# Optimization experiments

Hardware: AMD Instinct MI355X
Metric: run time of the kernel (lower is better)

Reference implementation:

```python
import jax, jax.numpy as jnp
import numpy as np

EPS = 1e-06


def setup_inputs() -> dict:
    key = jax.random.key(0)
    k1, k2 = jax.random.split(key)
    N, M, D = 8192, 8192, 512
    first_vector = jax.random.normal(k1, (N, D), dtype=jnp.float32)
    second_vector = jax.random.normal(k2, (M, D), dtype=jnp.float32)
    return {"first_vector": first_vector, "second_vector": second_vector, "normalize": 1}


def reference(first_vector, second_vector, normalize):
    # Pairwise dot products: [N, M]. Mathematically identical to the
    # broadcast multiply + sum over D in the torch module, but as a GEMM.
    sim = jnp.einsum('nd,md->nm', first_vector, second_vector)
    if normalize:
        # Note: module divides by sqrt(|a| * |b|) + eps (geometric mean of
        # norms, not the product) -- reproduce exactly.
        n1 = jnp.linalg.norm(first_vector, axis=1)[:, None]   # [N, 1]
        n2 = jnp.linalg.norm(second_vector, axis=1)[None, :]  # [1, M]
        sim = sim / (jnp.sqrt(n1 * n2) + EPS)
    return sim
```

## Files before the change

kernel.cpp:

```cpp
#include <hip/hip_runtime.h>
#include <hip/hip_bf16.h>
#include <math.h>

#define EPS 1e-6f

constexpr int D  = 512;
constexpr int BM = 256;
constexpr int BN = 256;

typedef __attribute__((ext_vector_type(8))) short  short8;
typedef __attribute__((ext_vector_type(4))) float  floatx4;

__device__ inline unsigned short f2bf(float f) {
  union { __hip_bfloat16 h; unsigned short u; } cvt;
  cvt.h = __float2bfloat16(f);
  return cvt.u;
}

__global__ __launch_bounds__(256) void prep_kernel(
    const float* __restrict__ src, __hip_bfloat16* __restrict__ dst,
    float* __restrict__ isn, int nrows) {
  const int lane = threadIdx.x & 63;
  const int row  = blockIdx.x * 4 + (threadIdx.x >> 6);
  if (row >= nrows) return;

  const float4* p4 = (const float4*)(src + (size_t)row * D);
  const float4 v1 = p4[lane];
  const float4 v2 = p4[lane + 64];

  if (dst != nullptr) {
    ushort4 u1, u2;
    u1.x = f2bf(v1.x); u1.y = f2bf(v1.y); u1.z = f2bf(v1.z); u1.w = f2bf(v1.w);
    u2.x = f2bf(v2.x); u2.y = f2bf(v2.y); u2.z = f2bf(v2.z); u2.w = f2bf(v2.w);
    ushort4* drow = (ushort4*)(dst + (size_t)row * D);
    drow[lane]      = u1;
    drow[lane + 64] = u2;
  }

  float ss = v1.x * v1.x + v1.y * v1.y + v1.z * v1.z + v1.w * v1.w
           + v2.x * v2.x + v2.y * v2.y + v2.z * v2.z + v2.w * v2.w;
  #pragma unroll
  for (int o = 32; o > 0; o >>= 1) ss += __shfl_down(ss, o);
  if (lane == 0) {
    const float n1 = sqrtf(ss);
    isn[row] = 1.0f / sqrtf(n1);
  }
}


#define GLD(srcp, ldsoff_shorts)                                              \
  __builtin_amdgcn_global_load_lds(                                           \
      (const __attribute__((address_space(1))) void*)(srcp),                  \
      (__attribute__((address_space(3))) void*)(smem + (ldsoff_shorts)),      \
      16, 0, 0)

#define STAGE_HALF(gbase, lbase)                                              \
  do {                                                                        \
    GLD((gbase) + soff,                   (lbase) + t * 8);                   \
    GLD((gbase) + soff + (size_t)64 * D,  (lbase) + (t + 512) * 8);           \
  } while (0)

#define STAGE_KTILE(kt, b)                                                    \
  do {                                                                        \
    STAGE_HALF(gA + (kt) * 64,                   ((b) * 2 + 0) * 8192);       \
    STAGE_HALF(gA + (kt) * 64 + (size_t)128 * D, ((b) * 2 + 1) * 8192);       \
    STAGE_HALF(gB + (kt) * 64,                   32768 + ((b) * 2 + 0) * 8192); \
    STAGE_HALF(gB + (kt) * 64 + (size_t)128 * D, 32768 + ((b) * 2 + 1) * 8192); \
  } while (0)

#define RD(p, m, off) (*(const short8*)((p) + (m) * 2048 + rbyte + (off)))

#define MM2(mi, ni)                                                           \
  do {                                                                        \
    acc[mi][ni] = __builtin_amdgcn_mfma_f32_16x16x32_bf16(                    \
        aR[(mi) & 3][0], bR[ni][0], acc[mi][ni], 0, 0, 0);                    \
    acc[mi][ni] = __builtin_amdgcn_mfma_f32_16x16x32_bf16(                    \
        aR[(mi) & 3][1], bR[ni][1], acc[mi][ni], 0, 0, 0);                    \
  } while (0)

#define BAR   __builtin_amdgcn_s_barrier()
#define LGKM0 do { asm volatile("s_waitcnt lgkmcnt(0)" ::: "memory");         \
                   __builtin_amdgcn_sched_barrier(0); } while (0)
#define VM8   asm volatile("s_waitcnt vmcnt(8)" ::: "memory")
#define VM0   asm volatile("s_waitcnt vmcnt(0)" ::: "memory")
#define NOOP  do {} while (0)

#define KTILE(b, STAGE_STMT, WAITV)                                           \
  do {                                                                        \
    const char* pA_ = (const char*)smem + ((b) * 2 + wm) * 16384;             \
    const char* pB_ = (const char*)smem + 65536                               \
                      + ((b) * 2 + (wn >> 1)) * 16384 + (wn & 1) * 8192;      \
                                 \
    aR[0][0] = RD(pA_, 0, off0); aR[0][1] = RD(pA_, 0, off1);                 \
    aR[1][0] = RD(pA_, 1, off0); aR[1][1] = RD(pA_, 1, off1);                 \
    aR[2][0] = RD(pA_, 2, off0); aR[2][1] = RD(pA_, 2, off1);                 \
    aR[3][0] = RD(pA_, 3, off0); aR[3][1] = RD(pA_, 3, off1);                 \
    bR[0][0] = RD(pB_, 0, off0); bR[0][1] = RD(pB_, 0, off1);                 \
    bR[1][0] = RD(pB_, 1, off0); bR[1][1] = RD(pB_, 1, off1);                 \
    BAR; LGKM0;                                                               \
    __builtin_amdgcn_s_setprio(1);                                            \
    MM2(0,0); MM2(1,0); MM2(2,0); MM2(3,0);                                   \
    MM2(0,1); MM2(1,1); MM2(2,1); MM2(3,1);                                   \
    __builtin_amdgcn_s_setprio(0);                                            \
    BAR;                                                                      \
                                                              \
    bR[2][0] = RD(pB_, 2, off0); bR[2][1] = RD(pB_, 2, off1);                 \
    bR[3][0] = RD(pB_, 3, off0); bR[3][1] = RD(pB_, 3, off1);                 \
    BAR; LGKM0;                                                               \
    __builtin_amdgcn_s_setprio(1);                                            \
    MM2(0,2); MM2(1,2); MM2(2,2); MM2(3,2);                                   \
    MM2(0,3); MM2(1,3); MM2(2,3); MM2(3,3);                                   \
    __builtin_amdgcn_s_setprio(0);                                            \
    BAR;                                                                      \
                                               \
    aR[0][0] = RD(pA_, 4, off0); aR[0][1] = RD(pA_, 4, off1);                 \
    aR[1][0] = RD(pA_, 5, off0); aR[1][1] = RD(pA_, 5, off1);                 \
    aR[2][0] = RD(pA_, 6, off0); aR[2][1] = RD(pA_, 6, off1);                 \
    aR[3][0] = RD(pA_, 7, off0); aR[3][1] = RD(pA_, 7, off1);                 \
    BAR; LGKM0;                                                               \
    __builtin_amdgcn_s_setprio(1);                                            \
    MM2(4,2); MM2(5,2); MM2(6,2); MM2(7,2);                                   \
    MM2(4,3); MM2(5,3); MM2(6,3); MM2(7,3);                                   \
    __builtin_amdgcn_s_setprio(0);                                            \
    BAR;                                                                      \
       \
    STAGE_STMT;                                                               \
    BAR;                                                                      \
    __builtin_amdgcn_s_setprio(1);                                            \
    MM2(4,0); MM2(5,0); MM2(6,0); MM2(7,0);                                   \
    MM2(4,1); MM2(5,1); MM2(6,1); MM2(7,1);                                   \
    __builtin_amdgcn_s_setprio(0);                                            \
    WAITV;                                                                    \
    BAR;                                                                      \
  } while (0)

__global__ __launch_bounds__(512, 2) void gemm256_kernel(
    const __hip_bfloat16* __restrict__ A, const __hip_bfloat16* __restrict__ B,
    const float* __restrict__ ia, const float* __restrict__ ib,
    const int* __restrict__ nrmflag, float* __restrict__ C,
    int N, int M) {
  __shared__ __align__(128) short smem[65536];

  const int t    = threadIdx.x;
  const int lane = t & 63;
  const int w    = t >> 6;
  const int wm   = w >> 2;
  const int wn   = w & 3;

  int bid = blockIdx.y * gridDim.x + blockIdx.x;
  const int nwg = (int)(gridDim.x * gridDim.y);
  if ((nwg & 7) == 0) bid = (bid & 7) * (nwg >> 3) + (bid >> 3);
  const int ix = bid % (int)gridDim.x;
  const int iy = bid / (int)gridDim.x;
  const size_t rowA0 = (size_t)ix * BM;
  const size_t rowB0 = (size_t)iy * BN;

  const int srow  = t >> 3;
  const int sslot = (t & 7) ^ (srow & 7);
  const size_t soff = (size_t)srow * D + sslot * 8;
  const unsigned short* gA = (const unsigned short*)A + rowA0 * D;
  const unsigned short* gB = (const unsigned short*)B + rowB0 * D;

  const int fr    = lane & 15;
  const int g4    = lane >> 4;
  const int rbyte = fr * 128;
  const int off0  = ((g4    ) ^ (fr & 7)) * 16;
  const int off1  = ((g4 + 4) ^ (fr & 7)) * 16;

  floatx4 acc[8][4];
  #pragma unroll
  for (int i = 0; i < 8; ++i)
    #pragma unroll
    for (int j = 0; j < 4; ++j) acc[i][j] = (floatx4){0.f, 0.f, 0.f, 0.f};

  short8 aR[4][2], bR[4][2];

  STAGE_KTILE(0, 0);
  STAGE_KTILE(1, 1);
  VM8;
  BAR;

  #pragma unroll
  for (int it = 0; it < 4; ++it) {
    if (it < 3) {
      KTILE(0, STAGE_KTILE(it * 2 + 2, 0), VM8);
      KTILE(1, STAGE_KTILE(it * 2 + 3, 1), VM8);
    } else {
      KTILE(0, NOOP, VM0);
      KTILE(1, NOOP, NOOP);
    }
  }

  const int nrm = *nrmflag;
  const int cq  = lane >> 4;
  const int cc  = lane & 15;

  float ibv[4];
  #pragma unroll
  for (int n = 0; n < 4; ++n)
    ibv[n] = nrm ? ib[rowB0 + wn * 64 + n * 16 + cc] : 1.0f;

  #pragma unroll
  for (int m = 0; m < 8; ++m) {
    const size_t rbase = rowA0 + wm * 128 + m * 16 + cq * 4;
    float4 iav4 = nrm ? *(const float4*)(ia + rbase) : (float4){1.f, 1.f, 1.f, 1.f};
    const float iavr[4] = {iav4.x, iav4.y, iav4.z, iav4.w};
    #pragma unroll
    for (int r = 0; r < 4; ++r) {
      float* crow = C + (rbase + r) * (size_t)M + rowB0 + wn * 64 + cc;
      #pragma unroll
      for (int n = 0; n < 4; ++n)
        crow[n * 16] = acc[m][n][r] * iavr[r] * ibv[n];
    }
  }
}

__global__ __launch_bounds__(256) void fb_gemm(
    const float* __restrict__ A, const float* __restrict__ B,
    const float* __restrict__ ia, const float* __restrict__ ib,
    const int* __restrict__ nrmflag, float* __restrict__ C, int N, int M) {
  __shared__ float sA[32][33];
  __shared__ float sB[32][33];
  const int tx = threadIdx.x & 31;
  const int ty = threadIdx.x >> 5;
  const size_t row0 = (size_t)blockIdx.y * 32;
  const size_t col0 = (size_t)blockIdx.x * 32;
  float acc[4] = {0.f, 0.f, 0.f, 0.f};
  for (int k0 = 0; k0 < D; k0 += 32) {
    #pragma unroll
    for (int r = 0; r < 4; ++r) {
      sA[ty + 8 * r][tx] = A[(row0 + ty + 8 * r) * D + k0 + tx];
      sB[ty + 8 * r][tx] = B[(col0 + ty + 8 * r) * D + k0 + tx];
    }
    __syncthreads();
    #pragma unroll 8
    for (int kk = 0; kk < 32; ++kk) {
      const float bv = sB[tx][kk];
      #pragma unroll
      for (int r = 0; r < 4; ++r) acc[r] += sA[ty + 8 * r][kk] * bv;
    }
    __syncthreads();
  }
  const int nrm  = *nrmflag;
  const float iv = ib[col0 + tx];
  #pragma unroll
  for (int r = 0; r < 4; ++r) {
    const size_t row = row0 + ty + 8 * r;
    float v = acc[r];
    if (nrm) {
      const float denom = 1.0f / (ia[row] * iv) + EPS;
      v /= denom;
    }
    C[row * (size_t)M + col0 + tx] = v;
  }
}

extern "C" void kernel_launch(void* const* d_in, const int* in_sizes, int n_in,
                              void* d_out, int out_size, void* d_ws, size_t ws_size,
                              hipStream_t stream) {
  const float* A   = (const float*)d_in[0];
  const float* B   = (const float*)d_in[1];
  const int*   nrm = (const int*)d_in[2];
  float*       C   = (float*)d_out;
  const int N = in_sizes[0] / D;
  const int M = in_sizes[1] / D;

  float* iaN = (float*)d_ws;
  float* ibN = iaN + N;
  __hip_bfloat16* Abf = (__hip_bfloat16*)(ibN + M);
  __hip_bfloat16* Bbf = Abf + (size_t)N * D;

  const size_t need = (size_t)(N + M) * sizeof(float)
                    + (size_t)(N + M) * D * sizeof(__hip_bfloat16);
  const bool fast = (ws_size >= need) && (N % BM == 0) && (M % BN == 0);

  prep_kernel<<<(N + 3) / 4, 256, 0, stream>>>(A, fast ? Abf : nullptr, iaN, N);
  prep_kernel<<<(M + 3) / 4, 256, 0, stream>>>(B, fast ? Bbf : nullptr, ibN, M);

  if (fast) {
    gemm256_kernel<<<dim3(N / BM, M / BN), 512, 0, stream>>>(Abf, Bbf, iaN, ibN, nrm, C, N, M);
  } else {
    fb_gemm<<<dim3(M / 32, N / 32), 256, 0, stream>>>(A, B, iaN, ibN, nrm, C, N, M);
  }
}
```

Measured before the change: 370.8 us.

## Persist GEMM blocks over four column tiles and fold norm scaling into bf16 prep

Each workgroup now computes four consecutive 256x256 output tiles along the M dimension. It prefetches the next tile's first k-slices during the tail of the current tile, which hides the pipeline fill and drain between tiles and reduces the grid size. The inverse-sqrt-norm scaling is applied to the bf16 operands in the prep kernel, so the GEMM epilogue becomes plain nontemporal stores with no ia/ib loads or multiplies. Pre-scaling before rounding to bf16 slightly changes numerics, and the launch has 4x fewer workgroups, which could under-fill the CUs.

```diff
diff --git a/kernel.cpp b/kernel.cpp
--- a/kernel.cpp
+++ b/kernel.cpp
@@ -4,9 +4,10 @@
 
 #define EPS 1e-6f
 
-constexpr int D  = 512;
-constexpr int BM = 256;
-constexpr int BN = 256;
+constexpr int D   = 512;
+constexpr int BM  = 256;
+constexpr int BN  = 256;
+constexpr int TPB = 4;
 
 typedef __attribute__((ext_vector_type(8))) short  short8;
 typedef __attribute__((ext_vector_type(4))) float  floatx4;
@@ -19,7 +20,7 @@
 
 __global__ __launch_bounds__(256) void prep_kernel(
     const float* __restrict__ src, __hip_bfloat16* __restrict__ dst,
-    float* __restrict__ isn, int nrows) {
+    float* __restrict__ isn, const int* __restrict__ nrmflag, int nrows) {
   const int lane = threadIdx.x & 63;
   const int row  = blockIdx.x * 4 + (threadIdx.x >> 6);
   if (row >= nrows) return;
@@ -28,22 +29,24 @@
   const float4 v1 = p4[lane];
   const float4 v2 = p4[lane + 64];
 
+  float ss = v1.x * v1.x + v1.y * v1.y + v1.z * v1.z + v1.w * v1.w
+           + v2.x * v2.x + v2.y * v2.y + v2.z * v2.z + v2.w * v2.w;
+  #pragma unroll
+  for (int o = 32; o > 0; o >>= 1) ss += __shfl_xor(ss, o);
+
+  const float s4 = rsqrtf(sqrtf(ss));
+  if (lane == 0) isn[row] = s4;
+
   if (dst != nullptr) {
+    const float s = (*nrmflag) ? s4 : 1.0f;
     ushort4 u1, u2;
-    u1.x = f2bf(v1.x); u1.y = f2bf(v1.y); u1.z = f2bf(v1.z); u1.w = f2bf(v1.w);
-    u2.x = f2bf(v2.x); u2.y = f2bf(v2.y); u2.z = f2bf(v2.z); u2.w = f2bf(v2.w);
+    u1.x = f2bf(v1.x * s); u1.y = f2bf(v1.y * s);
+    u1.z = f2bf(v1.z * s); u1.w = f2bf(v1.w * s);
+    u2.x = f2bf(v2.x * s); u2.y = f2bf(v2.y * s);
+    u2.z = f2bf(v2.z * s); u2.w = f2bf(v2.w * s);
     ushort4* drow = (ushort4*)(dst + (size_t)row * D);
     drow[lane]      = u1;
     drow[lane + 64] = u2;
-  }
-
-  float ss = v1.x * v1.x + v1.y * v1.y + v1.z * v1.z + v1.w * v1.w
-           + v2.x * v2.x + v2.y * v2.y + v2.z * v2.z + v2.w * v2.w;
-  #pragma unroll
-  for (int o = 32; o > 0; o >>= 1) ss += __shfl_down(ss, o);
-  if (lane == 0) {
-    const float n1 = sqrtf(ss);
-    isn[row] = 1.0f / sqrtf(n1);
   }
 }
 
@@ -54,18 +57,16 @@
       (__attribute__((address_space(3))) void*)(smem + (ldsoff_shorts)),      \
       16, 0, 0)
 
-#define STAGE_HALF(gbase, lbase)                                              \
-  do {                                                                        \
-    GLD((gbase) + soff,                   (lbase) + t * 8);                   \
-    GLD((gbase) + soff + (size_t)64 * D,  (lbase) + (t + 512) * 8);           \
-  } while (0)
-
-#define STAGE_KTILE(kt, b)                                                    \
-  do {                                                                        \
-    STAGE_HALF(gA + (kt) * 64,                   ((b) * 2 + 0) * 8192);       \
-    STAGE_HALF(gA + (kt) * 64 + (size_t)128 * D, ((b) * 2 + 1) * 8192);       \
-    STAGE_HALF(gB + (kt) * 64,                   32768 + ((b) * 2 + 0) * 8192); \
-    STAGE_HALF(gB + (kt) * 64 + (size_t)128 * D, 32768 + ((b) * 2 + 1) * 8192); \
+#define STAGE(aP, bP, b)                                                      \
+  do {                                                                        \
+    GLD((aP) + soff,                   ((b) * 2 + 0) * 8192 + t * 8);         \
+    GLD((aP) + soff + (size_t)64 * D,  ((b) * 2 + 0) * 8192 + (t + 512) * 8); \
+    GLD((aP) + soff + (size_t)128 * D, ((b) * 2 + 1) * 8192 + t * 8);         \
+    GLD((aP) + soff + (size_t)192 * D, ((b) * 2 + 1) * 8192 + (t + 512) * 8); \
+    GLD((bP) + soff,                   32768 + ((b) * 2 + 0) * 8192 + t * 8); \
+    GLD((bP) + soff + (size_t)64 * D,  32768 + ((b) * 2 + 0) * 8192 + (t + 512) * 8); \
+    GLD((bP) + soff + (size_t)128 * D, 32768 + ((b) * 2 + 1) * 8192 + t * 8); \
+    GLD((bP) + soff + (size_t)192 * D, 32768 + ((b) * 2 + 1) * 8192 + (t + 512) * 8); \
   } while (0)
 
 #define RD(p, m, off) (*(const short8*)((p) + (m) * 2048 + rbyte + (off)))
@@ -90,7 +91,7 @@
     const char* pA_ = (const char*)smem + ((b) * 2 + wm) * 16384;             \
     const char* pB_ = (const char*)smem + 65536                               \
                       + ((b) * 2 + (wn >> 1)) * 16384 + (wn & 1) * 8192;      \
-                                 \
+                                                     \
     aR[0][0] = RD(pA_, 0, off0); aR[0][1] = RD(pA_, 0, off1);                 \
     aR[1][0] = RD(pA_, 1, off0); aR[1][1] = RD(pA_, 1, off1);                 \
     aR[2][0] = RD(pA_, 2, off0); aR[2][1] = RD(pA_, 2, off1);                 \
@@ -112,7 +113,7 @@
     MM2(0,3); MM2(1,3); MM2(2,3); MM2(3,3);                                   \
     __builtin_amdgcn_s_setprio(0);                                            \
     BAR;                                                                      \
-                                               \
+                                                              \
     aR[0][0] = RD(pA_, 4, off0); aR[0][1] = RD(pA_, 4, off1);                 \
     aR[1][0] = RD(pA_, 5, off0); aR[1][1] = RD(pA_, 5, off1);                 \
     aR[2][0] = RD(pA_, 6, off0); aR[2][1] = RD(pA_, 6, off1);                 \
@@ -123,7 +124,7 @@
     MM2(4,3); MM2(5,3); MM2(6,3); MM2(7,3);                                   \
     __builtin_amdgcn_s_setprio(0);                                            \
     BAR;                                                                      \
-       \
+                            \
     STAGE_STMT;                                                               \
     BAR;                                                                      \
     __builtin_amdgcn_s_setprio(1);                                            \
@@ -134,11 +135,36 @@
     BAR;                                                                      \
   } while (0)
 
+#define TILE8(bBp, LASTP0, LASTP1, WV0, WV1)                                  \
+  do {                                                                        \
+    KTILE(0, STAGE(gA + 128, (bBp) + 128, 0), VM8);                           \
+    KTILE(1, STAGE(gA + 192, (bBp) + 192, 1), VM8);                           \
+    KTILE(0, STAGE(gA + 256, (bBp) + 256, 0), VM8);                           \
+    KTILE(1, STAGE(gA + 320, (bBp) + 320, 1), VM8);                           \
+    KTILE(0, STAGE(gA + 384, (bBp) + 384, 0), VM8);                           \
+    KTILE(1, STAGE(gA + 448, (bBp) + 448, 1), VM8);                           \
+    KTILE(0, LASTP0, WV0);                                                    \
+    KTILE(1, LASTP1, WV1);                                                    \
+  } while (0)
+
+#define EPILOGUE(col0_)                                                       \
+  do {                                                                        \
+    _Pragma("unroll")                                                         \
+    for (int m = 0; m < 8; ++m) {                                             \
+      const size_t rbase = rowA0 + wm * 128 + m * 16 + cq * 4;                \
+      _Pragma("unroll")                                                       \
+      for (int r = 0; r < 4; ++r) {                                           \
+        float* crow = C + (rbase + r) * (size_t)M + (col0_) + wn * 64 + cc;   \
+        _Pragma("unroll")                                                     \
+        for (int n = 0; n < 4; ++n)                                           \
+          __builtin_nontemporal_store(acc[m][n][r], crow + n * 16);           \
+      }                                                                       \
+    }                                                                         \
+  } while (0)
+
 __global__ __launch_bounds__(512, 2) void gemm256_kernel(
-    const __hip_bfloat16* __restrict__ A, const __hip_bfloat16* __restrict__ B,
-    const float* __restrict__ ia, const float* __restrict__ ib,
-    const int* __restrict__ nrmflag, float* __restrict__ C,
-    int N, int M) {
+    const __hip_bfloat16* __restrict__ Abf, const __hip_bfloat16* __restrict__ Bbf,
+    float* __restrict__ C, int N, int M) {
   __shared__ __align__(128) short smem[65536];
 
   const int t    = threadIdx.x;
@@ -147,72 +173,58 @@
   const int wm   = w >> 2;
   const int wn   = w & 3;
 
-  int bid = blockIdx.y * gridDim.x + blockIdx.x;
-  const int nwg = (int)(gridDim.x * gridDim.y);
-  if ((nwg & 7) == 0) bid = (bid & 7) * (nwg >> 3) + (bid >> 3);
-  const int ix = bid % (int)gridDim.x;
-  const int iy = bid / (int)gridDim.x;
-  const size_t rowA0 = (size_t)ix * BM;
-  const size_t rowB0 = (size_t)iy * BN;
+  const int nbx = N / BM;
+  const int nwg = (int)gridDim.x;
+  int lb = (int)blockIdx.x;
+  if ((nwg & 7) == 0) lb = (lb & 7) * (nwg >> 3) + (lb >> 3);
+  const int ix  = lb % nbx;
+  const int iyg = lb / nbx;
+
+  const size_t rowA0  = (size_t)ix * BM;
+  const size_t rowB00 = (size_t)iyg * (BN * TPB);
+  const unsigned short* gA  = (const unsigned short*)Abf + rowA0 * D;
+  const unsigned short* gB0 = (const unsigned short*)Bbf + rowB00 * D;
 
   const int srow  = t >> 3;
   const int sslot = (t & 7) ^ (srow & 7);
   const size_t soff = (size_t)srow * D + sslot * 8;
-  const unsigned short* gA = (const unsigned short*)A + rowA0 * D;
-  const unsigned short* gB = (const unsigned short*)B + rowB0 * D;
 
   const int fr    = lane & 15;
   const int g4    = lane >> 4;
   const int rbyte = fr * 128;
   const int off0  = ((g4    ) ^ (fr & 7)) * 16;
   const int off1  = ((g4 + 4) ^ (fr & 7)) * 16;
+  const int cq    = lane >> 4;
+  const int cc    = lane & 15;
 
   floatx4 acc[8][4];
+  short8 aR[4][2], bR[4][2];
+
+  STAGE(gA,      gB0,      0);
+  STAGE(gA + 64, gB0 + 64, 1);
+  VM8;
+  BAR;
+
+  const unsigned short* bB = gB0;
+  #pragma unroll 1
+  for (int tt = 0; tt < TPB - 1; ++tt) {
+    #pragma unroll
+    for (int i = 0; i < 8; ++i)
+      #pragma unroll
+      for (int j = 0; j < 4; ++j) acc[i][j] = (floatx4){0.f, 0.f, 0.f, 0.f};
+
+    const unsigned short* bBN = bB + BN * D;
+    TILE8(bB, STAGE(gA, bBN, 0), STAGE(gA + 64, bBN + 64, 1), VM8, VM8);
+    EPILOGUE(rowB00 + (size_t)tt * BN);
+    bB = bBN;
+  }
+
   #pragma unroll
   for (int i = 0; i < 8; ++i)
     #pragma unroll
     for (int j = 0; j < 4; ++j) acc[i][j] = (floatx4){0.f, 0.f, 0.f, 0.f};
-
-  short8 aR[4][2], bR[4][2];
-
-  STAGE_KTILE(0, 0);
-  STAGE_KTILE(1, 1);
-  VM8;
-  BAR;
-
-  #pragma unroll
-  for (int it = 0; it < 4; ++it) {
-    if (it < 3) {
-      KTILE(0, STAGE_KTILE(it * 2 + 2, 0), VM8);
-      KTILE(1, STAGE_KTILE(it * 2 + 3, 1), VM8);
-    } else {
-      KTILE(0, NOOP, VM0);
-      KTILE(1, NOOP, NOOP);
-    }
-  }
-
-  const int nrm = *nrmflag;
-  const int cq  = lane >> 4;
-  const int cc  = lane & 15;
-
-  float ibv[4];
-  #pragma unroll
-  for (int n = 0; n < 4; ++n)
-    ibv[n] = nrm ? ib[rowB0 + wn * 64 + n * 16 + cc] : 1.0f;
-
-  #pragma unroll
-  for (int m = 0; m < 8; ++m) {
-    const size_t rbase = rowA0 + wm * 128 + m * 16 + cq * 4;
-    float4 iav4 = nrm ? *(const float4*)(ia + rbase) : (float4){1.f, 1.f, 1.f, 1.f};
-    const float iavr[4] = {iav4.x, iav4.y, iav4.z, iav4.w};
-    #pragma unroll
-    for (int r = 0; r < 4; ++r) {
-      float* crow = C + (rbase + r) * (size_t)M + rowB0 + wn * 64 + cc;
-      #pragma unroll
-      for (int n = 0; n < 4; ++n)
-        crow[n * 16] = acc[m][n][r] * iavr[r] * ibv[n];
-    }
-  }
+  TILE8(bB, NOOP, NOOP, VM0, NOOP);
+  EPILOGUE(rowB00 + (size_t)(TPB - 1) * BN);
 }
 
 __global__ __launch_bounds__(256) void fb_gemm(
@@ -272,13 +284,14 @@
 
   const size_t need = (size_t)(N + M) * sizeof(float)
                     + (size_t)(N + M) * D * sizeof(__hip_bfloat16);
-  const bool fast = (ws_size >= need) && (N % BM == 0) && (M % BN == 0);
-
-  prep_kernel<<<(N + 3) / 4, 256, 0, stream>>>(A, fast ? Abf : nullptr, iaN, N);
-  prep_kernel<<<(M + 3) / 4, 256, 0, stream>>>(B, fast ? Bbf : nullptr, ibN, M);
+  const bool fast = (ws_size >= need) && (N % BM == 0) && (M % (BN * TPB) == 0);
+
+  prep_kernel<<<(N + 3) / 4, 256, 0, stream>>>(A, fast ? Abf : nullptr, iaN, nrm, N);
+  prep_kernel<<<(M + 3) / 4, 256, 0, stream>>>(B, fast ? Bbf : nullptr, ibN, nrm, M);
 
   if (fast) {
-    gemm256_kernel<<<dim3(N / BM, M / BN), 512, 0, stream>>>(Abf, Bbf, iaN, ibN, nrm, C, N, M);
+    const int nwg = (N / BM) * (M / (BN * TPB));
+    gemm256_kernel<<<dim3(nwg), 512, 0, stream>>>(Abf, Bbf, C, N, M);
   } else {
     fb_gemm<<<dim3(M / 32, N / 32), 256, 0, stream>>>(A, B, iaN, ibN, nrm, C, N, M);
   }
```

After: 389.2 us. 4.9% more time.
